# Kernel tuning notes

Hardware: AMD Instinct MI355X
Metric: run time of the kernel (lower is better)

Reference implementation:

```python
import jax, jax.numpy as jnp
import numpy as np
import math

MU = 5; ETA = 1.0; ITERS = 3
SIGMA_C = 1.0; SIGMA_S = 1.6 * SIGMA_C
SIGMA_M = 3.0; RHO = 0.99; TAU = 0.7
MAX_T = int(math.floor(3 * SIGMA_C))  # 3
MAX_S = int(math.floor(3 * SIGMA_M))  # 9
DELTA = 1.0
B, C, X, Y = 4, 1, 512, 512


def _gpdf(v, sig):
    return math.exp(-v * v / (2.0 * sig * sig)) / (math.sqrt(2.0 * math.pi) * sig)


def _sobel(img):
    k = jnp.array([[-1., -2., -1.], [0., 0., 0.], [1., 2., 1.]], dtype=img.dtype)
    kern = jnp.stack([k, k.T])[:, None]  # [2,1,3,3] OIHW
    return jax.lax.conv_general_dilated(img, kern, (1, 1), [(1, 1), (1, 1)],
                                        dimension_numbers=('NCHW', 'OIHW', 'NCHW'))


def _gather_flat(arr, idx):
    # arr [b,c,x,y], idx int [b,x,y] flattened spatial index (px*Y+py)
    b, c, x, y = arr.shape
    flat = arr.reshape(b, c, x * y)
    idxb = jnp.broadcast_to(idx.reshape(b, 1, x * y), (b, c, x * y))
    return jnp.take_along_axis(flat, idxb, axis=2).reshape(b, c, x, y)


def _safe_norm(v):
    m = jnp.linalg.norm(v, axis=1, keepdims=True)
    return v / jnp.where(m == 0, 1.0, m)


def _etf(images):
    b, c, x, y = images.shape
    sob = _sobel(images)                                   # [b,2,x,y]
    mag = jnp.linalg.norm(sob, axis=1, keepdims=True)      # [b,1,x,y]
    mag = mag / jnp.max(mag)
    mag_p = jnp.pad(mag, ((0, 0), (0, 0), (MU, MU), (MU, MU)))
    sobel_X = mag[:, None]                                 # [b,1,1,x,y]
    tang = _safe_norm(jnp.stack([-sob[:, 1], sob[:, 0]], axis=1))
    K = 2 * MU + 1
    for _ in range(ITERS):
        for ori in ('V', 'H'):
            tang_p = jnp.pad(tang, ((0, 0), (0, 0), (MU, MU), (MU, MU)))
            tang_X = tang[:, None]                         # [b,1,2,x,y]
            if ori == 'V':
                tang_Y = jnp.stack([tang_p[:, :, i:i + x, MU:MU + y] for i in range(K)], axis=1)
                sobel_Y = jnp.stack([mag_p[:, :, i:i + x, MU:MU + y] for i in range(K)], axis=1)
            else:
                tang_Y = jnp.stack([tang_p[:, :, MU:MU + x, i:i + y] for i in range(K)], axis=1)
                sobel_Y = jnp.stack([mag_p[:, :, MU:MU + x, i:i + y] for i in range(K)], axis=1)
            # weight: magnitude term * direction term / 2
            w = (jnp.tanh(ETA * (sobel_Y - sobel_X)) + 1.0) \
                * jnp.sum(tang_X * tang_Y, axis=2, keepdims=True) * 0.5
            tang = _safe_norm(jnp.sum(tang_Y * w, axis=1))
    return tang


def _dog(images, etf):
    b, c, x, y = images.shape
    xi, yi = jnp.meshgrid(jnp.arange(x, dtype=images.dtype),
                          jnp.arange(y, dtype=images.dtype), indexing='ij')
    idx0 = jnp.broadcast_to(jnp.stack([xi, yi])[None], (b, 2, x, y))
    per = jnp.stack([-etf[:, 1], etf[:, 0]], axis=1)       # perpendicular to flow
    dog = jnp.zeros_like(images)
    tw = 0.0
    for t in range(-MAX_T, MAX_T + 1):
        pts = idx0 + DELTA * per * t
        px = jnp.round(jnp.clip(pts[:, 0], 0, x - 1)).astype(jnp.int32)
        py = jnp.round(jnp.clip(pts[:, 1], 0, y - 1)).astype(jnp.int32)
        il = _gather_flat(images, px * y + py)
        gw = _gpdf(t, SIGMA_C) - RHO * _gpdf(t, SIGMA_S)
        tw += gw
        dog = dog + il * gw
    return dog / tw


def _fdog_float(images):
    b, c, x, y = images.shape
    etf = _etf(images)
    dog = _dog(images, etf)
    fdog = jnp.zeros_like(images)
    tw = 0.0
    xi, yi = jnp.meshgrid(jnp.arange(x, dtype=jnp.int32),
                          jnp.arange(y, dtype=jnp.int32), indexing='ij')
    for s_dir in (-1, 1):
        px = jnp.broadcast_to(xi[None], (b, x, y))
        py = jnp.broadcast_to(yi[None], (b, x, y))
        for s in range(0 if s_dir == 1 else 1, MAX_S + 1):
            if s != 0:
                p_etf = _gather_flat(etf, px * y + py)     # flow at current points
                fx = px.astype(images.dtype) + DELTA * p_etf[:, 0] * s_dir
                fy = py.astype(images.dtype) + DELTA * p_etf[:, 1] * s_dir
                px = jnp.round(jnp.clip(fx, 0, x - 1)).astype(jnp.int32)
                py = jnp.round(jnp.clip(fy, 0, y - 1)).astype(jnp.int32)
            f_s = _gather_flat(dog, px * y + py)
            gw = _gpdf(s, SIGMA_M)
            tw += gw
            fdog = fdog + f_s * gw
    return fdog / tw


def setup_inputs() -> dict:
    key = jax.random.key(0)
    images = jax.random.uniform(key, (B, C, X, Y), dtype=jnp.float32)
    return {"images": images}


def reference(images):
    fdog = _fdog_float(images)
    edges = ~((fdog < 0) & (1.0 + jnp.tanh(fdog) < TAU))
    return edges.astype(jnp.int32)
```

## Files before the change

kernel.cpp:

```cpp
#include <hip/hip_runtime.h>
#include <math.h>

#pragma clang fp contract(off)

#define BN 4
#define SX 512
#define SY 512
#define NPIX (BN * SX * SY)
#define MU 5
#define MB (1024 * 1024)
#define NBLOCKS 4096

struct DogW  { float g[7];  float tw; };
struct FdogW { float g[10]; float tw; };

__device__ __forceinline__ float fast_tanh_f32(float dF) {
    double d = (double)dF;
    double y = fabs(d);
    double t = expm1(2.0 * y);
    double r = t / (t + 2.0);
    if (y > 350.0) r = 1.0;
    return (float)copysign(r, d);
}

__device__ __forceinline__ float img_at(const float* __restrict__ img, int b, int x, int y) {
    if (x < 0 || x >= SX || y < 0 || y >= SY) return 0.0f;
    return img[(size_t)b * SX * SY + (size_t)x * SY + y];
}

__global__ void k_sobel(const float* __restrict__ img, float* __restrict__ mag,
                        float2* __restrict__ tang, float* __restrict__ partial) {
#pragma clang fp contract(off)
    int yi = blockIdx.x * blockDim.x + threadIdx.x;
    int xi = blockIdx.y;
    int b  = blockIdx.z;

    float v00 = img_at(img, b, xi - 1, yi - 1);
    float v01 = img_at(img, b, xi - 1, yi    );
    float v02 = img_at(img, b, xi - 1, yi + 1);
    float v10 = img_at(img, b, xi,     yi - 1);
    float v12 = img_at(img, b, xi,     yi + 1);
    float v20 = img_at(img, b, xi + 1, yi - 1);
    float v21 = img_at(img, b, xi + 1, yi    );
    float v22 = img_at(img, b, xi + 1, yi + 1);

    float s0 = (-1.0f * v00);
    s0 = s0 + (-2.0f * v01);
    s0 = s0 + (-1.0f * v02);
    s0 = s0 + ( 1.0f * v20);
    s0 = s0 + ( 2.0f * v21);
    s0 = s0 + ( 1.0f * v22);
    float s1 = (-1.0f * v00);
    s1 = s1 + ( 1.0f * v02);
    s1 = s1 + (-2.0f * v10);
    s1 = s1 + ( 2.0f * v12);
    s1 = s1 + (-1.0f * v20);
    s1 = s1 + ( 1.0f * v22);

    float m = sqrtf((s0 * s0) + (s1 * s1));
    size_t idx = (size_t)b * SX * SY + (size_t)xi * SY + yi;
    mag[idx] = m;

    float tx = -s1, ty = s0;
    float n = sqrtf((tx * tx) + (ty * ty));
    float d = (n == 0.0f) ? 1.0f : n;
    tang[idx] = make_float2(tx / d, ty / d);

    float wm = m;
    for (int off = 32; off > 0; off >>= 1) wm = fmaxf(wm, __shfl_down(wm, off, 64));
    __shared__ float red[4];
    int lane = threadIdx.x & 63;
    int wid  = threadIdx.x >> 6;
    if (lane == 0) red[wid] = wm;
    __syncthreads();
    if (threadIdx.x == 0) {
        float bm = fmaxf(fmaxf(red[0], red[1]), fmaxf(red[2], red[3]));
        int bid = blockIdx.x + gridDim.x * (blockIdx.y + gridDim.y * blockIdx.z);
        partial[bid] = bm;
    }
}

__global__ void k_reduce(const float* __restrict__ partial, unsigned int* __restrict__ maxbits) {
    float m = 0.0f;
    for (int i = threadIdx.x; i < NBLOCKS; i += 256) m = fmaxf(m, partial[i]);
    for (int off = 32; off > 0; off >>= 1) m = fmaxf(m, __shfl_down(m, off, 64));
    __shared__ float red[4];
    int lane = threadIdx.x & 63;
    int wid  = threadIdx.x >> 6;
    if (lane == 0) red[wid] = m;
    __syncthreads();
    if (threadIdx.x == 0) {
        float bm = fmaxf(fmaxf(red[0], red[1]), fmaxf(red[2], red[3]));
        *maxbits = __float_as_uint(bm);
    }
}

__global__ void k_norm(float* __restrict__ mag, const unsigned int* __restrict__ maxbits) {
    int i = blockIdx.x * blockDim.x + threadIdx.x;
    float mx = __uint_as_float(*maxbits);
    mag[i] = mag[i] / mx;
}

__global__ void k_tanh(const float* __restrict__ mag, const unsigned int* __restrict__ maxbits,
                       float* __restrict__ TV, float* __restrict__ TH) {
#pragma clang fp contract(off)
    int yi = blockIdx.x * blockDim.x + threadIdx.x;
    int xi = blockIdx.y;
    int b  = blockIdx.z;
    size_t base = (size_t)b * SX * SY;
    size_t idx  = base + (size_t)xi * SY + yi;
    float mx = __uint_as_float(*maxbits);
    float cm = mag[idx] / mx;
#pragma unroll
    for (int k = 1; k <= 5; ++k) {
        if (xi + k < SX) {
            float nm = mag[idx + (size_t)k * SY] / mx;
            TV[(size_t)(k - 1) * NPIX + idx] = fast_tanh_f32(nm - cm);
        }
    }
#pragma unroll
    for (int k = 1; k <= 5; ++k) {
        if (yi + k < SY) {
            float nm = mag[idx + k] / mx;
            TH[(size_t)(k - 1) * NPIX + idx] = fast_tanh_f32(nm - cm);
        }
    }
}

#define VTY 32
#define VTX 8
__global__ __launch_bounds__(256) void k_etf_v(const float2* __restrict__ tsrc,
                                               float2* __restrict__ tdst,
                                               const float* __restrict__ TV) {
#pragma clang fp contract(off)
    int ty = threadIdx.x & 31;
    int tx = threadIdx.x >> 5;
    int y0 = blockIdx.x * VTY;
    int x0 = blockIdx.y * VTX;
    int b  = blockIdx.z;
    size_t base = (size_t)b * SX * SY;

    __shared__ __align__(16) float2 sT[VTX + 2 * MU][VTY];
    __shared__ __align__(16) float  sTV[5][VTX + MU][VTY];

    int tid = threadIdx.x;
    for (int i = tid; i < (VTX + 2 * MU) * (VTY / 2) / 2; i += 256) {
        break;
    }
    for (int i = tid; i < (VTX + 2 * MU) * (VTY / 4) * 2; i += 256) {
        int r = i >> 4;
        int c = i & 15;
        int gx = x0 - MU + r;
        if (gx >= 0 && gx < SX)
            ((float4*)&sT[r][0])[c] = ((const float4*)(tsrc + base + (size_t)gx * SY + y0))[c];
    }
    for (int i = tid; i < 5 * (VTX + MU) * (VTY / 4); i += 256) {
        int j   = i / ((VTX + MU) * (VTY / 4));
        int rem = i - j * ((VTX + MU) * (VTY / 4));
        int r   = rem >> 3;
        int c   = rem & 7;
        int gx  = x0 - MU + r;
        if (gx >= 0 && gx < SX)
            ((float4*)&sTV[j][r][0])[c] =
                ((const float4*)(TV + (size_t)j * NPIX + base + (size_t)gx * SY + y0))[c];
    }
    __syncthreads();

    int xi = x0 + tx;
    int yi = y0 + ty;
    size_t idx = base + (size_t)xi * SY + yi;

    float2 ct = sT[tx + MU][ty];

    float sx = 0.0f, sy = 0.0f;
#pragma unroll
    for (int k = -MU; k <= MU; ++k) {
        int nx = xi + k;
        if (nx < 0 || nx >= SX) continue;
        float2 nt = sT[tx + MU + k][ty];
        float th;
        if (k > 0)      th =  sTV[k - 1][tx + MU][ty];
        else if (k < 0) th = -sTV[-k - 1][tx + MU + k][ty];
        else            th =  0.0f;
        float dot = (ct.x * nt.x) + (ct.y * nt.y);
        float w   = ((th + 1.0f) * dot) * 0.5f;
        sx = sx + (nt.x * w);
        sy = sy + (nt.y * w);
    }
    float n = sqrtf((sx * sx) + (sy * sy));
    float d = (n == 0.0f) ? 1.0f : n;
    tdst[idx] = make_float2(sx / d, sy / d);
}

__global__ __launch_bounds__(256) void k_etf_h(const float2* __restrict__ tsrc,
                                               float2* __restrict__ tdst,
                                               const float* __restrict__ TH) {
#pragma clang fp contract(off)
    int tid = threadIdx.x;
    int xi  = blockIdx.y;
    int b   = blockIdx.z;
    size_t rowbase = (size_t)b * SX * SY + (size_t)xi * SY;

    __shared__ __align__(16) float2 sT[SY];
    __shared__ __align__(16) float  sTH[5][SY];

    ((float4*)sT)[tid] = ((const float4*)(tsrc + rowbase))[tid];
    for (int i = tid; i < 5 * (SY / 4); i += 256) {
        int j = i >> 7;
        int c = i & 127;
        ((float4*)&sTH[0][0])[i] = ((const float4*)(TH + (size_t)j * NPIX + rowbase))[c];
    }
    __syncthreads();

#pragma unroll
    for (int half = 0; half < 2; ++half) {
        int yi = tid + half * 256;
        float2 ct = sT[yi];
        float sx = 0.0f, sy = 0.0f;
#pragma unroll
        for (int k = -MU; k <= MU; ++k) {
            int ny = yi + k;
            if (ny < 0 || ny >= SY) continue;
            float2 nt = sT[ny];
            float th;
            if (k > 0)      th =  sTH[k - 1][yi];
            else if (k < 0) th = -sTH[-k - 1][ny];
            else            th =  0.0f;
            float dot = (ct.x * nt.x) + (ct.y * nt.y);
            float w   = ((th + 1.0f) * dot) * 0.5f;
            sx = sx + (nt.x * w);
            sy = sy + (nt.y * w);
        }
        float n = sqrtf((sx * sx) + (sy * sy));
        float d = (n == 0.0f) ? 1.0f : n;
        tdst[rowbase + yi] = make_float2(sx / d, sy / d);
    }
}

__global__ void k_etf(const float2* __restrict__ tsrc, float2* __restrict__ tdst,
                      const float* __restrict__ mag, int vert) {
#pragma clang fp contract(off)
    int yi = blockIdx.x * blockDim.x + threadIdx.x;
    int xi = blockIdx.y;
    int b  = blockIdx.z;
    size_t base = (size_t)b * SX * SY;
    size_t idx  = base + (size_t)xi * SY + yi;

    float  cm = mag[idx];
    float2 ct = tsrc[idx];

    float sx = 0.0f, sy = 0.0f;
    for (int k = -MU; k <= MU; ++k) {
        int nx = xi + (vert ? k : 0);
        int ny = yi + (vert ? 0 : k);
        if (nx < 0 || nx >= SX || ny < 0 || ny >= SY) continue;
        size_t nidx = base + (size_t)nx * SY + ny;
        float  nm = mag[nidx];
        float2 nt = tsrc[nidx];
        float dot = (ct.x * nt.x) + (ct.y * nt.y);
        float th  = (float)tanh((double)(nm - cm));
        float w   = ((th + 1.0f) * dot) * 0.5f;
        sx = sx + (nt.x * w);
        sy = sy + (nt.y * w);
    }
    float n = sqrtf((sx * sx) + (sy * sy));
    float d = (n == 0.0f) ? 1.0f : n;
    tdst[idx] = make_float2(sx / d, sy / d);
}

__global__ void k_dog(const float* __restrict__ img, const float2* __restrict__ etf,
                      float* __restrict__ dog, DogW w) {
#pragma clang fp contract(off)
    int yi = blockIdx.x * blockDim.x + threadIdx.x;
    int xi = blockIdx.y;
    int b  = blockIdx.z;
    size_t base = (size_t)b * SX * SY;
    size_t idx  = base + (size_t)xi * SY + yi;

    float2 e = etf[idx];
    float perx = -e.y;
    float pery =  e.x;
    float xf = (float)xi, yf = (float)yi;

    float acc = 0.0f;
#pragma unroll
    for (int t = -3; t <= 3; ++t) {
        float tf  = (float)t;
        float ptx = xf + (perx * tf);
        float pty = yf + (pery * tf);
        int px = (int)rintf(fminf(fmaxf(ptx, 0.0f), (float)(SX - 1)));
        int py = (int)rintf(fminf(fmaxf(pty, 0.0f), (float)(SY - 1)));
        float il = img[base + (size_t)px * SY + py];
        acc = acc + (il * w.g[t + 3]);
    }
    dog[idx] = acc / w.tw;
}

__global__ void k_fdog(const float* __restrict__ dog, const float2* __restrict__ etf,
                       int* __restrict__ out, FdogW w) {
#pragma clang fp contract(off)
    int yi = blockIdx.x * blockDim.x + threadIdx.x;
    int xi = blockIdx.y;
    int b  = blockIdx.z;
    size_t base = (size_t)b * SX * SY;
    size_t idx  = base + (size_t)xi * SY + yi;

    float d1[9];
    float d2[10];
    float2 e0 = etf[idx];
    float2 e1 = e0, e2 = e0;
    int p1x = xi, p1y = yi;
    int p2x = xi, p2y = yi;
    d2[0] = dog[idx];

#pragma unroll
    for (int s = 1; s <= 9; ++s) {
        float fx1 = (float)p1x + (e1.x * -1.0f);
        float fy1 = (float)p1y + (e1.y * -1.0f);
        p1x = (int)rintf(fminf(fmaxf(fx1, 0.0f), (float)(SX - 1)));
        p1y = (int)rintf(fminf(fmaxf(fy1, 0.0f), (float)(SY - 1)));
        size_t i1 = base + (size_t)p1x * SY + p1y;
        float fx2 = (float)p2x + (e2.x * 1.0f);
        float fy2 = (float)p2y + (e2.y * 1.0f);
        p2x = (int)rintf(fminf(fmaxf(fx2, 0.0f), (float)(SX - 1)));
        p2y = (int)rintf(fminf(fmaxf(fy2, 0.0f), (float)(SY - 1)));
        size_t i2 = base + (size_t)p2x * SY + p2y;

        d1[s - 1] = dog[i1];
        d2[s]     = dog[i2];
        if (s < 9) {
            e1 = etf[i1];
            e2 = etf[i2];
        }
    }

    float acc = 0.0f;
#pragma unroll
    for (int s = 1; s <= 9; ++s) acc = acc + (d1[s - 1] * w.g[s]);
    acc = acc + (d2[0] * w.g[0]);
#pragma unroll
    for (int s = 1; s <= 9; ++s) acc = acc + (d2[s] * w.g[s]);

    float fv = acc / w.tw;
    float th = 1.0f + fast_tanh_f32(fv);
    out[idx] = ((fv < 0.0f) && (th < 0.7f)) ? 0 : 1;
}

static double gpdf(double v, double sig) {
    return exp(-(v * v) / (2.0 * sig * sig)) / (sqrt(2.0 * M_PI) * sig);
}

extern "C" void kernel_launch(void* const* d_in, const int* in_sizes, int n_in,
                              void* d_out, int out_size, void* d_ws, size_t ws_size,
                              hipStream_t stream) {
    const float* img = (const float*)d_in[0];
    int* out = (int*)d_out;
    char* ws = (char*)d_ws;

    const size_t need = (size_t)60 * MB + NBLOCKS * sizeof(float) + 4;
    bool fast = ws_size >= need;

    float*  mag = (float*)(ws);
    float2* tA  = (float2*)(ws + (size_t)4  * MB);
    float2* tB  = (float2*)(ws + (size_t)12 * MB);
    float*  dog = (float*)(ws + (size_t)12 * MB);
    float*  TV  = (float*)(ws + (size_t)20 * MB);
    float*  TH  = (float*)(ws + (size_t)40 * MB);
    size_t  tail = fast ? (size_t)60 * MB : (size_t)20 * MB;
    float*        partial = (float*)(ws + tail);
    unsigned int* maxbits = (unsigned int*)(ws + tail + NBLOCKS * sizeof(float));

    dim3 blk(256, 1, 1);
    dim3 grd(SY / 256, SX, BN);
    dim3 vgrd(SY / VTY, SX / VTX, BN);
    dim3 hgrd(1, SX, BN);

    k_sobel<<<grd, blk, 0, stream>>>(img, mag, tA, partial);
    k_reduce<<<1, 256, 0, stream>>>(partial, maxbits);

    float2* src = tA;
    float2* dst = tB;
    if (fast) {
        k_tanh<<<grd, blk, 0, stream>>>(mag, maxbits, TV, TH);
        for (int it = 0; it < 3; ++it) {
            k_etf_v<<<vgrd, blk, 0, stream>>>(src, dst, TV);
            { float2* t = src; src = dst; dst = t; }
            k_etf_h<<<hgrd, blk, 0, stream>>>(src, dst, TH);
            { float2* t = src; src = dst; dst = t; }
        }
    } else {
        k_norm<<<NPIX / 256, 256, 0, stream>>>(mag, maxbits);
        for (int it = 0; it < 3; ++it) {
            k_etf<<<grd, blk, 0, stream>>>(src, dst, mag, 1);
            { float2* t = src; src = dst; dst = t; }
            k_etf<<<grd, blk, 0, stream>>>(src, dst, mag, 0);
            { float2* t = src; src = dst; dst = t; }
        }
    }
    float* dogbuf = (src == tA) ? dog : (float*)tA;

    DogW dw;
    {
        double tw = 0.0;
        for (int t = -3; t <= 3; ++t) {
            double g = gpdf((double)t, 1.0) - 0.99 * gpdf((double)t, 1.6);
            dw.g[t + 3] = (float)g;
            tw += g;
        }
        dw.tw = (float)tw;
    }
    k_dog<<<grd, blk, 0, stream>>>(img, src, dogbuf, dw);

    FdogW fw;
    {
        for (int s = 0; s <= 9; ++s) fw.g[s] = (float)gpdf((double)s, 3.0);
        double tw = 0.0;
        for (int s = 1; s <= 9; ++s) tw += gpdf((double)s, 3.0);
        for (int s = 0; s <= 9; ++s) tw += gpdf((double)s, 3.0);
        fw.tw = (float)tw;
    }
    k_fdog<<<grd, blk, 0, stream>>>(dogbuf, src, out, fw);
}
```

Baseline: 195.6 us.

## Fuse DoG into last ETF pass, atomic max reduction, taller vertical tiles

Replaces the two-pass max reduction with a per-block atomicMax on float bits after a memset, which removes the k_reduce launch. Computes the DoG directly inside the final horizontal ETF pass and writes it into the mag buffer, dropping the separate k_dog launch and its re-read of the flow field. Grows the vertical ETF tile from 8 to 32 rows, with each thread handling 4 rows, so less of each tile is spent on halo reloads. The costs are extra work and scattered image gathers in the last horizontal pass, atomic contention across 4096 blocks, and reliance on the magnitudes being non-negative for the unsigned-bits max to be correct.

```diff
diff --git a/kernel.cpp b/kernel.cpp
--- a/kernel.cpp
+++ b/kernel.cpp
@@ -9,7 +9,6 @@
 #define NPIX (BN * SX * SY)
 #define MU 5
 #define MB (1024 * 1024)
-#define NBLOCKS 4096
 
 struct DogW  { float g[7];  float tw; };
 struct FdogW { float g[10]; float tw; };
@@ -29,7 +28,7 @@
 }
 
 __global__ void k_sobel(const float* __restrict__ img, float* __restrict__ mag,
-                        float2* __restrict__ tang, float* __restrict__ partial) {
+                        float2* __restrict__ tang, unsigned int* __restrict__ maxbits) {
 #pragma clang fp contract(off)
     int yi = blockIdx.x * blockDim.x + threadIdx.x;
     int xi = blockIdx.y;
@@ -75,23 +74,7 @@
     __syncthreads();
     if (threadIdx.x == 0) {
         float bm = fmaxf(fmaxf(red[0], red[1]), fmaxf(red[2], red[3]));
-        int bid = blockIdx.x + gridDim.x * (blockIdx.y + gridDim.y * blockIdx.z);
-        partial[bid] = bm;
-    }
-}
-
-__global__ void k_reduce(const float* __restrict__ partial, unsigned int* __restrict__ maxbits) {
-    float m = 0.0f;
-    for (int i = threadIdx.x; i < NBLOCKS; i += 256) m = fmaxf(m, partial[i]);
-    for (int off = 32; off > 0; off >>= 1) m = fmaxf(m, __shfl_down(m, off, 64));
-    __shared__ float red[4];
-    int lane = threadIdx.x & 63;
-    int wid  = threadIdx.x >> 6;
-    if (lane == 0) red[wid] = m;
-    __syncthreads();
-    if (threadIdx.x == 0) {
-        float bm = fmaxf(fmaxf(red[0], red[1]), fmaxf(red[2], red[3]));
-        *maxbits = __float_as_uint(bm);
+        atomicMax(maxbits, __float_as_uint(bm));
     }
 }
 
@@ -128,13 +111,13 @@
 }
 
 #define VTY 32
-#define VTX 8
+#define VTX 32
 __global__ __launch_bounds__(256) void k_etf_v(const float2* __restrict__ tsrc,
                                                float2* __restrict__ tdst,
                                                const float* __restrict__ TV) {
 #pragma clang fp contract(off)
-    int ty = threadIdx.x & 31;
-    int tx = threadIdx.x >> 5;
+    int ty  = threadIdx.x & 31;
+    int txw = threadIdx.x >> 5;
     int y0 = blockIdx.x * VTY;
     int x0 = blockIdx.y * VTX;
     int b  = blockIdx.z;
@@ -144,9 +127,6 @@
     __shared__ __align__(16) float  sTV[5][VTX + MU][VTY];
 
     int tid = threadIdx.x;
-    for (int i = tid; i < (VTX + 2 * MU) * (VTY / 2) / 2; i += 256) {
-        break;
-    }
     for (int i = tid; i < (VTX + 2 * MU) * (VTY / 4) * 2; i += 256) {
         int r = i >> 4;
         int c = i & 15;
@@ -166,40 +146,47 @@
     }
     __syncthreads();
 
-    int xi = x0 + tx;
     int yi = y0 + ty;
-    size_t idx = base + (size_t)xi * SY + yi;
-
-    float2 ct = sT[tx + MU][ty];
-
-    float sx = 0.0f, sy = 0.0f;
-#pragma unroll
-    for (int k = -MU; k <= MU; ++k) {
-        int nx = xi + k;
-        if (nx < 0 || nx >= SX) continue;
-        float2 nt = sT[tx + MU + k][ty];
-        float th;
-        if (k > 0)      th =  sTV[k - 1][tx + MU][ty];
-        else if (k < 0) th = -sTV[-k - 1][tx + MU + k][ty];
-        else            th =  0.0f;
-        float dot = (ct.x * nt.x) + (ct.y * nt.y);
-        float w   = ((th + 1.0f) * dot) * 0.5f;
-        sx = sx + (nt.x * w);
-        sy = sy + (nt.y * w);
-    }
-    float n = sqrtf((sx * sx) + (sy * sy));
-    float d = (n == 0.0f) ? 1.0f : n;
-    tdst[idx] = make_float2(sx / d, sy / d);
+#pragma unroll
+    for (int sub = 0; sub < 4; ++sub) {
+        int tx = txw + (sub << 3);
+        int xi = x0 + tx;
+        size_t idx = base + (size_t)xi * SY + yi;
+
+        float2 ct = sT[tx + MU][ty];
+        float sx = 0.0f, sy = 0.0f;
+#pragma unroll
+        for (int k = -MU; k <= MU; ++k) {
+            int nx = xi + k;
+            if (nx < 0 || nx >= SX) continue;
+            float2 nt = sT[tx + MU + k][ty];
+            float th;
+            if (k > 0)      th =  sTV[k - 1][tx + MU][ty];
+            else if (k < 0) th = -sTV[-k - 1][tx + MU + k][ty];
+            else            th =  0.0f;
+            float dot = (ct.x * nt.x) + (ct.y * nt.y);
+            float w   = ((th + 1.0f) * dot) * 0.5f;
+            sx = sx + (nt.x * w);
+            sy = sy + (nt.y * w);
+        }
+        float n = sqrtf((sx * sx) + (sy * sy));
+        float d = (n == 0.0f) ? 1.0f : n;
+        tdst[idx] = make_float2(sx / d, sy / d);
+    }
 }
 
 __global__ __launch_bounds__(256) void k_etf_h(const float2* __restrict__ tsrc,
                                                float2* __restrict__ tdst,
-                                               const float* __restrict__ TH) {
+                                               const float* __restrict__ TH,
+                                               const float* __restrict__ img,
+                                               float* __restrict__ dogout,
+                                               DogW dw, int do_dog) {
 #pragma clang fp contract(off)
     int tid = threadIdx.x;
     int xi  = blockIdx.y;
     int b   = blockIdx.z;
-    size_t rowbase = (size_t)b * SX * SY + (size_t)xi * SY;
+    size_t base    = (size_t)b * SX * SY;
+    size_t rowbase = base + (size_t)xi * SY;
 
     __shared__ __align__(16) float2 sT[SY];
     __shared__ __align__(16) float  sTH[5][SY];
@@ -233,7 +220,27 @@
         }
         float n = sqrtf((sx * sx) + (sy * sy));
         float d = (n == 0.0f) ? 1.0f : n;
-        tdst[rowbase + yi] = make_float2(sx / d, sy / d);
+        float ex = sx / d;
+        float ey = sy / d;
+        tdst[rowbase + yi] = make_float2(ex, ey);
+
+        if (do_dog) {
+            float perx = -ey;
+            float pery =  ex;
+            float xf = (float)xi, yf = (float)yi;
+            float acc = 0.0f;
+#pragma unroll
+            for (int t = -3; t <= 3; ++t) {
+                float tf  = (float)t;
+                float ptx = xf + (perx * tf);
+                float pty = yf + (pery * tf);
+                int px = (int)rintf(fminf(fmaxf(ptx, 0.0f), (float)(SX - 1)));
+                int py = (int)rintf(fminf(fmaxf(pty, 0.0f), (float)(SY - 1)));
+                float il = img[base + (size_t)px * SY + py];
+                acc = acc + (il * dw.g[t + 3]);
+            }
+            dogout[rowbase + yi] = acc / dw.tw;
+        }
     }
 }
 
@@ -357,37 +364,56 @@
     int* out = (int*)d_out;
     char* ws = (char*)d_ws;
 
-    const size_t need = (size_t)60 * MB + NBLOCKS * sizeof(float) + 4;
+    const size_t need = (size_t)60 * MB + 4;
     bool fast = ws_size >= need;
 
     float*  mag = (float*)(ws);
     float2* tA  = (float2*)(ws + (size_t)4  * MB);
     float2* tB  = (float2*)(ws + (size_t)12 * MB);
-    float*  dog = (float*)(ws + (size_t)12 * MB);
     float*  TV  = (float*)(ws + (size_t)20 * MB);
     float*  TH  = (float*)(ws + (size_t)40 * MB);
     size_t  tail = fast ? (size_t)60 * MB : (size_t)20 * MB;
-    float*        partial = (float*)(ws + tail);
-    unsigned int* maxbits = (unsigned int*)(ws + tail + NBLOCKS * sizeof(float));
+    unsigned int* maxbits = (unsigned int*)(ws + tail);
 
     dim3 blk(256, 1, 1);
     dim3 grd(SY / 256, SX, BN);
     dim3 vgrd(SY / VTY, SX / VTX, BN);
     dim3 hgrd(1, SX, BN);
 
-    k_sobel<<<grd, blk, 0, stream>>>(img, mag, tA, partial);
-    k_reduce<<<1, 256, 0, stream>>>(partial, maxbits);
+    DogW dw;
+    {
+        double tw = 0.0;
+        for (int t = -3; t <= 3; ++t) {
+            double g = gpdf((double)t, 1.0) - 0.99 * gpdf((double)t, 1.6);
+            dw.g[t + 3] = (float)g;
+            tw += g;
+        }
+        dw.tw = (float)tw;
+    }
+    FdogW fw;
+    {
+        for (int s = 0; s <= 9; ++s) fw.g[s] = (float)gpdf((double)s, 3.0);
+        double tw = 0.0;
+        for (int s = 1; s <= 9; ++s) tw += gpdf((double)s, 3.0);
+        for (int s = 0; s <= 9; ++s) tw += gpdf((double)s, 3.0);
+        fw.tw = (float)tw;
+    }
+
+    hipMemsetAsync(maxbits, 0, sizeof(unsigned int), stream);
+    k_sobel<<<grd, blk, 0, stream>>>(img, mag, tA, maxbits);
 
     float2* src = tA;
     float2* dst = tB;
     if (fast) {
+        float* dogbuf = mag;
         k_tanh<<<grd, blk, 0, stream>>>(mag, maxbits, TV, TH);
         for (int it = 0; it < 3; ++it) {
             k_etf_v<<<vgrd, blk, 0, stream>>>(src, dst, TV);
             { float2* t = src; src = dst; dst = t; }
-            k_etf_h<<<hgrd, blk, 0, stream>>>(src, dst, TH);
+            k_etf_h<<<hgrd, blk, 0, stream>>>(src, dst, TH, img, dogbuf, dw, it == 2);
             { float2* t = src; src = dst; dst = t; }
         }
+        k_fdog<<<grd, blk, 0, stream>>>(dogbuf, src, out, fw);
     } else {
         k_norm<<<NPIX / 256, 256, 0, stream>>>(mag, maxbits);
         for (int it = 0; it < 3; ++it) {
@@ -396,28 +422,8 @@
             k_etf<<<grd, blk, 0, stream>>>(src, dst, mag, 0);
             { float2* t = src; src = dst; dst = t; }
         }
-    }
-    float* dogbuf = (src == tA) ? dog : (float*)tA;
-
-    DogW dw;
-    {
-        double tw = 0.0;
-        for (int t = -3; t <= 3; ++t) {
-            double g = gpdf((double)t, 1.0) - 0.99 * gpdf((double)t, 1.6);
-            dw.g[t + 3] = (float)g;
-            tw += g;
-        }
-        dw.tw = (float)tw;
-    }
-    k_dog<<<grd, blk, 0, stream>>>(img, src, dogbuf, dw);
-
-    FdogW fw;
-    {
-        for (int s = 0; s <= 9; ++s) fw.g[s] = (float)gpdf((double)s, 3.0);
-        double tw = 0.0;
-        for (int s = 1; s <= 9; ++s) tw += gpdf((double)s, 3.0);
-        for (int s = 0; s <= 9; ++s) tw += gpdf((double)s, 3.0);
-        fw.tw = (float)tw;
-    }
-    k_fdog<<<grd, blk, 0, stream>>>(dogbuf, src, out, fw);
-}
+        float* dogbuf = (src == tA) ? (float*)tB : (float*)tA;
+        k_dog<<<grd, blk, 0, stream>>>(img, src, dogbuf, dw);
+        k_fdog<<<grd, blk, 0, stream>>>(dogbuf, src, out, fw);
+    }
+}
```

New measurement: 235.9 us. 1.21x slower.
